# Optimization experiments

Hardware: AMD Instinct MI355X
Metric: run time of the kernel (lower is better)

Reference implementation:

```python
import jax, jax.numpy as jnp
import numpy as np
from jax import lax

PAD_IDX = 0  # padding_index from init
B, T, E, H, V = 128, 24, 512, 512, 10000


def setup_inputs() -> dict:
    key = jax.random.key(0)
    ks = jax.random.split(key, 10)
    return {
        "images": jax.random.normal(ks[0], (B, H), jnp.float32),
        "captions": jax.random.randint(ks[1], (B, T), 0, V),
        "captions_length": jax.random.randint(ks[2], (B,), 1, T + 1),
        "W_emb": jax.random.normal(ks[3], (V, E), jnp.float32) * 0.02,
        "W_ih": jax.random.normal(ks[4], (4 * H, E), jnp.float32) * 0.02,
        "W_hh": jax.random.normal(ks[5], (4 * H, H), jnp.float32) * 0.02,
        "b_ih": jax.random.normal(ks[6], (4 * H,), jnp.float32) * 0.02,
        "b_hh": jax.random.normal(ks[7], (4 * H,), jnp.float32) * 0.02,
        "W_out": jax.random.normal(ks[8], (V, H), jnp.float32) * 0.02,
        "b_out": jax.random.normal(ks[9], (V,), jnp.float32) * 0.02,
    }


def reference(images, captions, captions_length, W_emb, W_ih, W_hh, b_ih, b_hh, W_out, b_out):
    # embedding with padding_idx: padding row forced to zero
    emb_table = W_emb.at[PAD_IDX].set(0.0)
    x = emb_table[captions]  # [B, T, E]
    bdim = images.shape[0]
    hdim = W_hh.shape[1]
    vocab = W_out.shape[0]
    bias = b_ih + b_hh

    def step(carry, xt):
        h, c = carry
        # PyTorch LSTMCell gate order: i, f, g, o
        gates = xt @ W_ih.T + h @ W_hh.T + bias  # [B, 4H]
        i, f, g, o = jnp.split(gates, 4, axis=-1)
        c = jax.nn.sigmoid(f) * c + jax.nn.sigmoid(i) * jnp.tanh(g)
        h = jax.nn.sigmoid(o) * jnp.tanh(c)
        logits = h @ W_out.T + b_out  # [B, V]
        return (h, c), logits

    c0 = jnp.zeros((bdim, hdim), images.dtype)
    _, ys = lax.scan(step, (images, c0), jnp.transpose(x, (1, 0, 2)))  # ys: [T, B, V]

    # deterministic <SOS>-like start output: one-hot at index 1, prepended at t=0
    start = jnp.zeros((vocab,), images.dtype).at[1].set(1.0)
    outputs = jnp.concatenate(
        [jnp.broadcast_to(start, (bdim, 1, vocab)), jnp.transpose(ys, (1, 0, 2))], axis=1
    )  # [B, T+1, V]
    return outputs, captions_length - 1
```

## Files before the change

kernel.cpp:

```cpp
#include <hip/hip_runtime.h>

constexpr int B_  = 128;
constexpr int T_  = 24;
constexpr int E_  = 512;
constexpr int H_  = 512;
constexpr int V_  = 10000;
constexpr int G4  = 2048;
constexpr int TP1 = 25;

typedef __attribute__((ext_vector_type(8))) short bf16x8;
typedef __attribute__((ext_vector_type(4))) short short4v;
typedef __attribute__((ext_vector_type(4))) float f32x4;

#define MFMA_16x16x32_BF16(a, b, c) __builtin_amdgcn_mfma_f32_16x16x32_bf16((a), (b), (c), 0, 0, 0)

__device__ inline unsigned short f2bf(float f) {
    unsigned int u = __float_as_uint(f);
    unsigned int r = (u + 0x7FFFu + ((u >> 16) & 1u)) >> 16;
    return (unsigned short)r;
}

__device__ inline void gl16(const unsigned short* g, unsigned short* l) {
    __builtin_amdgcn_global_load_lds(
        (const __attribute__((address_space(1))) unsigned int*)g,
        (__attribute__((address_space(3))) unsigned int*)l, 16, 0, 0);
}

__device__ inline int swz16(int row, int lq) {
    return (((row << 2) | lq) ^ (row & 7)) << 3;
}

__global__ __launch_bounds__(256) void k_prep(const float* __restrict__ Wih,
                                              const float* __restrict__ Whh,
                                              const float* __restrict__ Wout,
                                              const float* __restrict__ images,
                                              const float* __restrict__ Wemb,
                                              const int* __restrict__ captions,
                                              const int* __restrict__ cap_len,
                                              unsigned short* __restrict__ dWih,
                                              unsigned short* __restrict__ dWhh,
                                              unsigned short* __restrict__ dWout,
                                              unsigned short* __restrict__ dimg,
                                              unsigned short* __restrict__ Xemb,
                                              float* __restrict__ out,
                                              unsigned* __restrict__ flg) {
    int b = blockIdx.x;
    if (b == 0) flg[threadIdx.x * 32] = 0u;
    if (b < 7112) {
        const float* src; unsigned short* dst; int i;
        if (b < 1024)      { src = Wih;    dst = dWih;  i = b * 256 + threadIdx.x; }
        else if (b < 2048) { src = Whh;    dst = dWhh;  i = (b - 1024) * 256 + threadIdx.x; }
        else if (b < 7048) { src = Wout;   dst = dWout; i = (b - 2048) * 256 + threadIdx.x; }
        else               { src = images; dst = dimg;  i = (b - 7048) * 256 + threadIdx.x; }
        float4 v = ((const float4*)src)[i];
        short4v o;
        o[0] = (short)f2bf(v.x); o[1] = (short)f2bf(v.y);
        o[2] = (short)f2bf(v.z); o[3] = (short)f2bf(v.w);
        ((short4v*)dst)[i] = o;
    } else if (b < 8648) {
        int i = (b - 7112) * 256 + threadIdx.x;
        int row = i >> 7;
        int k4  = i & 127;
        int bb = row & 127, t = row >> 7;
        int tok = captions[bb * T_ + t];
        short4v o = {0, 0, 0, 0};
        if (tok > 0 && tok < V_) {
            float4 v = ((const float4*)(Wemb + (long)tok * E_))[k4];
            o[0] = (short)f2bf(v.x); o[1] = (short)f2bf(v.y);
            o[2] = (short)f2bf(v.z); o[3] = (short)f2bf(v.w);
        }
        ((short4v*)Xemb)[(long)row * 128 + k4] = o;
    } else {
        int idx = (b - 8648) * 256 + threadIdx.x;
        constexpr int Q = V_ / 4;
        if (idx < B_ * Q) {
            int bb = idx / Q;
            int q = idx - bb * Q;
            float4 zero = {0.f, 0.f, 0.f, 0.f};
            float4 one1 = {0.f, 1.f, 0.f, 0.f};
            ((float4*)out)[(long)bb * (TP1 * Q) + q] = (q == 0) ? one1 : zero;
        }
        if (idx < B_)
            out[(size_t)B_ * TP1 * V_ + idx] = (float)(cap_len[idx] - 1);
    }
}

__global__ __launch_bounds__(256, 1) void k_lstm(const unsigned short* __restrict__ Xemb,
                                                 const unsigned short* __restrict__ h0,
                                                 unsigned* __restrict__ hx0,
                                                 unsigned* __restrict__ hx1,
                                                 unsigned short* __restrict__ Hall,
                                                 const unsigned short* __restrict__ Whh,
                                                 const unsigned short* __restrict__ Wih,
                                                 const float* __restrict__ bih,
                                                 const float* __restrict__ bhh,
                                                 unsigned* __restrict__ flg) {
    __shared__ float part[16][4][64];
    int w    = threadIdx.x >> 6;
    int lane = threadIdx.x & 63;
    int lm = lane & 15, lq = lane >> 4;
    int MI = blockIdx.x >> 5;
    int HG = blockIdx.x & 31;
    int hcol = HG * 16 + lm;
    int ks = w * 128;
    int brow = MI * 16 + lq * 4 + w;
    unsigned* myFlg = flg + (MI * 32 + HG) * 32;
    unsigned* wFlg  = flg + (MI * 32 + (w << 3)) * 32;

    bf16x8 bw[4][4];
    bf16x8 wv[4][4];
    #pragma unroll
    for (int g = 0; g < 4; g++)
        #pragma unroll
        for (int kk = 0; kk < 4; kk++) {
            size_t off = (size_t)(g * 512 + hcol) * 512 + ks + kk * 32 + lq * 8;
            bw[g][kk] = *(const bf16x8*)((const short*)Whh + off);
            wv[g][kk] = *(const bf16x8*)((const short*)Wih + off);
        }

    float bs0 = bih[0 * 512 + hcol] + bhh[0 * 512 + hcol];
    float bs1 = bih[1 * 512 + hcol] + bhh[1 * 512 + hcol];
    float bs2 = bih[2 * 512 + hcol] + bhh[2 * 512 + hcol];
    float bs3 = bih[3 * 512 + hcol] + bhh[3 * 512 + hcol];

    float cp = 0.f;

    for (int t = 0; t < T_; t++) {
        const unsigned short* X = Xemb + ((size_t)(t * 128 + MI * 16 + lm)) * 512 + ks;
        bf16x8 xa[4];
        #pragma unroll
        for (int kk = 0; kk < 4; kk++)
            xa[kk] = *(const bf16x8*)(X + kk * 32 + lq * 8);

        f32x4 acc[4] = {};
        #pragma unroll
        for (int kk = 0; kk < 4; kk++) {
            acc[0] = MFMA_16x16x32_BF16(xa[kk], wv[0][kk], acc[0]);
            acc[1] = MFMA_16x16x32_BF16(xa[kk], wv[1][kk], acc[1]);
            acc[2] = MFMA_16x16x32_BF16(xa[kk], wv[2][kk], acc[2]);
            acc[3] = MFMA_16x16x32_BF16(xa[kk], wv[3][kk], acc[3]);
        }

        bf16x8 a[4];
        if (t == 0) {
            const unsigned short* A = h0 + (size_t)(MI * 16 + lm) * 512 + ks;
            #pragma unroll
            for (int kk = 0; kk < 4; kk++)
                a[kk] = *(const bf16x8*)(A + kk * 32 + lq * 8);
        } else {
            if (lane < 8) {
                unsigned want = (unsigned)t;
                while (__hip_atomic_load(wFlg + lane * 32, __ATOMIC_RELAXED,
                                         __HIP_MEMORY_SCOPE_AGENT) < want)
                    __builtin_amdgcn_s_sleep(1);
            }
            __builtin_amdgcn_wave_barrier();
            asm volatile("" ::: "memory");
            const unsigned long long* A = (const unsigned long long*)
                (((t & 1) ? hx1 : hx0) + ((size_t)(MI * 16 + lm) * 512 + ks) / 2);
            #pragma unroll
            for (int kk = 0; kk < 4; kk++) {
                union { unsigned long long q[2]; bf16x8 v; } cv;
                cv.q[0] = __hip_atomic_load(A + kk * 8 + lq * 2,
                                            __ATOMIC_RELAXED, __HIP_MEMORY_SCOPE_AGENT);
                cv.q[1] = __hip_atomic_load(A + kk * 8 + lq * 2 + 1,
                                            __ATOMIC_RELAXED, __HIP_MEMORY_SCOPE_AGENT);
                a[kk] = cv.v;
            }
        }

        #pragma unroll
        for (int kk = 0; kk < 4; kk++) {
            acc[0] = MFMA_16x16x32_BF16(a[kk], bw[0][kk], acc[0]);
            acc[1] = MFMA_16x16x32_BF16(a[kk], bw[1][kk], acc[1]);
            acc[2] = MFMA_16x16x32_BF16(a[kk], bw[2][kk], acc[2]);
            acc[3] = MFMA_16x16x32_BF16(a[kk], bw[3][kk], acc[3]);
        }

        #pragma unroll
        for (int g = 0; g < 4; g++)
            #pragma unroll
            for (int r = 0; r < 4; r++)
                part[g * 4 + r][w][lane] = acc[g][r];
        __syncthreads();

        float gi = part[0*4+w][0][lane] + part[0*4+w][1][lane] + part[0*4+w][2][lane] + part[0*4+w][3][lane] + bs0;
        float gf = part[1*4+w][0][lane] + part[1*4+w][1][lane] + part[1*4+w][2][lane] + part[1*4+w][3][lane] + bs1;
        float gg = part[2*4+w][0][lane] + part[2*4+w][1][lane] + part[2*4+w][2][lane] + part[2*4+w][3][lane] + bs2;
        float go = part[3*4+w][0][lane] + part[3*4+w][1][lane] + part[3*4+w][2][lane] + part[3*4+w][3][lane] + bs3;
        float si = 1.f / (1.f + expf(-gi));
        float sf = 1.f / (1.f + expf(-gf));
        float so = 1.f / (1.f + expf(-go));
        float cn = sf * cp + si * tanhf(gg);
        float hn = so * tanhf(cn);
        cp = cn;
        unsigned short hb = f2bf(hn);

        if (t < T_ - 1) {
            unsigned up = ((unsigned)(unsigned short)__shfl_down((int)hb, 1) << 16) | (unsigned)hb;
            unsigned* HW = (t & 1) ? hx0 : hx1;
            if (!(lm & 1))
                __hip_atomic_store(HW + (brow * 512 + hcol) / 2, up,
                                   __ATOMIC_RELAXED, __HIP_MEMORY_SCOPE_AGENT);
            asm volatile("s_waitcnt vmcnt(0)" ::: "memory");
            __syncthreads();
            if (threadIdx.x == 0)
                __hip_atomic_store(myFlg, (unsigned)(t + 1), __ATOMIC_RELAXED,
                                   __HIP_MEMORY_SCOPE_AGENT);
        }
        Hall[(size_t)t * (B_ * H_) + brow * 512 + hcol] = hb;
    }
}

__global__ __launch_bounds__(256) void k_logits(const unsigned short* __restrict__ Hall,
                                                const unsigned short* __restrict__ Wout,
                                                const float* __restrict__ bout,
                                                float* __restrict__ out) {
    __shared__ unsigned short ldsA[2][4096];
    __shared__ unsigned short ldsB[2][4096];
    int bid = blockIdx.x;
    int xcd = bid & 7;
    int q   = bid >> 3;
    int MI  = xcd * 3 + (q % 3);
    int NI  = q / 3;
    int i    = threadIdx.x;
    int w = i >> 6, lane = i & 63;
    int lm = lane & 15, lq = lane >> 4;
    int wr = w >> 1, wc = w & 1;

    int mm0 = ((i >> 2) & 7) ^ ((i >> 4) & 1);
    int li  = i ^ mm0;
    const unsigned short* gA = Hall + (size_t)(MI * 128 + (li >> 2)) * 512 + (li & 3) * 8;
    const unsigned short* gB = Wout + (size_t)(NI * 128 + (li >> 2)) * 512 + (li & 3) * 8;
    unsigned short* lA = &ldsA[0][0] + i * 8;
    unsigned short* lB = &ldsB[0][0] + i * 8;

    auto stage = [&](int buf, int ks) {
        int go = ks * 32;
        gl16(gA + go,            lA + buf * 4096);
        gl16(gA + go + 64 * 512, lA + buf * 4096 + 2048);
        gl16(gB + go,            lB + buf * 4096);
        gl16(gB + go + 64 * 512, lB + buf * 4096 + 2048);
    };

    f32x4 acc[4][4] = {};
    stage(0, 0);
    for (int ksi = 0; ksi < 16; ksi++) {
        int cur = ksi & 1;
        if (ksi < 15) stage(cur ^ 1, ksi + 1);
        __syncthreads();
        bf16x8 af[4], bfr[4];
        #pragma unroll
        for (int mi = 0; mi < 4; mi++)
            af[mi] = *(const bf16x8*)&ldsA[cur][swz16(wr * 64 + mi * 16 + lm, lq)];
        #pragma unroll
        for (int ni = 0; ni < 4; ni++)
            bfr[ni] = *(const bf16x8*)&ldsB[cur][swz16(wc * 64 + ni * 16 + lm, lq)];
        #pragma unroll
        for (int mi = 0; mi < 4; mi++)
            #pragma unroll
            for (int ni = 0; ni < 4; ni++)
                acc[mi][ni] = MFMA_16x16x32_BF16(af[mi], bfr[ni], acc[mi][ni]);
        __syncthreads();
    }

    #pragma unroll
    for (int mi = 0; mi < 4; mi++) {
        #pragma unroll
        for (int r = 0; r < 4; r++) {
            int b = wr * 64 + mi * 16 + lq * 4 + r;
            float* orow = out + ((size_t)b * TP1 + MI + 1) * V_;
            #pragma unroll
            for (int ni = 0; ni < 4; ni++) {
                int n = NI * 128 + wc * 64 + ni * 16 + lm;
                if (n < V_) orow[n] = acc[mi][ni][r] + bout[n];
            }
        }
    }
}

extern "C" void kernel_launch(void* const* d_in, const int* in_sizes, int n_in,
                              void* d_out, int out_size, void* d_ws, size_t ws_size,
                              hipStream_t stream) {
    const float* images   = (const float*)d_in[0];
    const int*   captions = (const int*)d_in[1];
    const int*   cap_len  = (const int*)d_in[2];
    const float* Wemb     = (const float*)d_in[3];
    const float* Wih      = (const float*)d_in[4];
    const float* Whh      = (const float*)d_in[5];
    const float* bih      = (const float*)d_in[6];
    const float* bhh      = (const float*)d_in[7];
    const float* Wout     = (const float*)d_in[8];
    const float* bout     = (const float*)d_in[9];
    float* out = (float*)d_out;

    char* ws = (char*)d_ws;
    unsigned short* Wih_bf  = (unsigned short*)(ws);
    unsigned short* Whh_bf  = (unsigned short*)(ws + 2097152);
    unsigned short* Wout_bf = (unsigned short*)(ws + 4194304);
    unsigned short* Xemb    = (unsigned short*)(ws + 14434304);
    unsigned short* Hall    = (unsigned short*)(ws + 17580032);
    unsigned short* h0      = (unsigned short*)(ws + 20725760);
    unsigned*       hx0     = (unsigned*)(ws + 20856832);
    unsigned*       hx1     = (unsigned*)(ws + 20987904);
    unsigned*       flg     = (unsigned*)(ws + 21118976);

    k_prep<<<9898, 256, 0, stream>>>(Wih, Whh, Wout, images, Wemb, captions,
                                     cap_len, Wih_bf, Whh_bf, Wout_bf, h0,
                                     Xemb, out, flg);

    k_lstm<<<256, 256, 0, stream>>>(Xemb, h0, hx0, hx1, Hall, Whh_bf, Wih_bf,
                                    bih, bhh, flg);

    k_logits<<<1896, 256, 0, stream>>>(Hall, Wout_bf, bout, out);
}
```

Baseline: 319.2 us.

## Replace per-block flag barrier with step-tagged hidden-state words

```diff
diff --git a/kernel.cpp b/kernel.cpp
--- a/kernel.cpp
+++ b/kernel.cpp
@@ -43,9 +43,8 @@
                                               unsigned short* __restrict__ dimg,
                                               unsigned short* __restrict__ Xemb,
                                               float* __restrict__ out,
-                                              unsigned* __restrict__ flg) {
+                                              unsigned long long* __restrict__ hq) {
     int b = blockIdx.x;
-    if (b == 0) flg[threadIdx.x * 32] = 0u;
     if (b < 7112) {
         const float* src; unsigned short* dst; int i;
         if (b < 1024)      { src = Wih;    dst = dWih;  i = b * 256 + threadIdx.x; }
@@ -70,7 +69,7 @@
             o[2] = (short)f2bf(v.z); o[3] = (short)f2bf(v.w);
         }
         ((short4v*)Xemb)[(long)row * 128 + k4] = o;
-    } else {
+    } else if (b < 9898) {
         int idx = (b - 8648) * 256 + threadIdx.x;
         constexpr int Q = V_ / 4;
         if (idx < B_ * Q) {
@@ -82,19 +81,21 @@
         }
         if (idx < B_)
             out[(size_t)B_ * TP1 * V_ + idx] = (float)(cap_len[idx] - 1);
+    } else {
+        int idx = (b - 9898) * 256 + threadIdx.x;
+        unsigned long long* p = hq + (size_t)idx * 4;
+        p[0] = 0ull; p[1] = 0ull; p[2] = 0ull; p[3] = 0ull;
     }
 }
 
 __global__ __launch_bounds__(256, 1) void k_lstm(const unsigned short* __restrict__ Xemb,
                                                  const unsigned short* __restrict__ h0,
-                                                 unsigned* __restrict__ hx0,
-                                                 unsigned* __restrict__ hx1,
+                                                 unsigned long long* __restrict__ hq,
                                                  unsigned short* __restrict__ Hall,
                                                  const unsigned short* __restrict__ Whh,
                                                  const unsigned short* __restrict__ Wih,
                                                  const float* __restrict__ bih,
-                                                 const float* __restrict__ bhh,
-                                                 unsigned* __restrict__ flg) {
+                                                 const float* __restrict__ bhh) {
     __shared__ float part[16][4][64];
     int w    = threadIdx.x >> 6;
     int lane = threadIdx.x & 63;
@@ -104,8 +105,6 @@
     int hcol = HG * 16 + lm;
     int ks = w * 128;
     int brow = MI * 16 + lq * 4 + w;
-    unsigned* myFlg = flg + (MI * 32 + HG) * 32;
-    unsigned* wFlg  = flg + (MI * 32 + (w << 3)) * 32;
 
     bf16x8 bw[4][4];
     bf16x8 wv[4][4];
@@ -148,23 +147,30 @@
             for (int kk = 0; kk < 4; kk++)
                 a[kk] = *(const bf16x8*)(A + kk * 32 + lq * 8);
         } else {
-            if (lane < 8) {
-                unsigned want = (unsigned)t;
-                while (__hip_atomic_load(wFlg + lane * 32, __ATOMIC_RELAXED,
-                                         __HIP_MEMORY_SCOPE_AGENT) < want)
-                    __builtin_amdgcn_s_sleep(1);
-            }
-            __builtin_amdgcn_wave_barrier();
-            asm volatile("" ::: "memory");
-            const unsigned long long* A = (const unsigned long long*)
-                (((t & 1) ? hx1 : hx0) + ((size_t)(MI * 16 + lm) * 512 + ks) / 2);
+            const unsigned long long* S = hq + (size_t)(t - 1) * 32768 +
+                (size_t)(MI * 16 + lm) * 256 + (ks >> 1) + lq * 4;
+            unsigned long long q[4][4];
+            #pragma unroll
+            for (int kk = 0; kk < 4; kk++)
+                #pragma unroll
+                for (int j = 0; j < 4; j++)
+                    q[kk][j] = __hip_atomic_load(S + kk * 16 + j,
+                                 __ATOMIC_RELAXED, __HIP_MEMORY_SCOPE_AGENT);
+            unsigned want = (unsigned)t;
+            #pragma unroll
+            for (int kk = 0; kk < 4; kk++)
+                #pragma unroll
+                for (int j = 0; j < 4; j++)
+                    while ((unsigned)(q[kk][j] >> 32) != want) {
+                        __builtin_amdgcn_s_sleep(1);
+                        q[kk][j] = __hip_atomic_load(S + kk * 16 + j,
+                                     __ATOMIC_RELAXED, __HIP_MEMORY_SCOPE_AGENT);
+                    }
             #pragma unroll
             for (int kk = 0; kk < 4; kk++) {
-                union { unsigned long long q[2]; bf16x8 v; } cv;
-                cv.q[0] = __hip_atomic_load(A + kk * 8 + lq * 2,
-                                            __ATOMIC_RELAXED, __HIP_MEMORY_SCOPE_AGENT);
-                cv.q[1] = __hip_atomic_load(A + kk * 8 + lq * 2 + 1,
-                                            __ATOMIC_RELAXED, __HIP_MEMORY_SCOPE_AGENT);
+                union { unsigned u[4]; bf16x8 v; } cv;
+                #pragma unroll
+                for (int j = 0; j < 4; j++) cv.u[j] = (unsigned)q[kk][j];
                 a[kk] = cv.v;
             }
         }
@@ -197,18 +203,17 @@
         unsigned short hb = f2bf(hn);
 
         if (t < T_ - 1) {
-            unsigned up = ((unsigned)(unsigned short)__shfl_down((int)hb, 1) << 16) | (unsigned)hb;
-            unsigned* HW = (t & 1) ? hx0 : hx1;
-            if (!(lm & 1))
-                __hip_atomic_store(HW + (brow * 512 + hcol) / 2, up,
+            unsigned hb1 = (unsigned short)__shfl_down((int)hb, 1);
+            if (!(lm & 1)) {
+                unsigned long long qv = ((unsigned long long)(unsigned)(t + 1) << 32)
+                                      | ((unsigned)hb | (hb1 << 16));
+                __hip_atomic_store(hq + (size_t)t * 32768 +
+                                   ((size_t)brow * 512 + hcol) / 2, qv,
                                    __ATOMIC_RELAXED, __HIP_MEMORY_SCOPE_AGENT);
-            asm volatile("s_waitcnt vmcnt(0)" ::: "memory");
-            __syncthreads();
-            if (threadIdx.x == 0)
-                __hip_atomic_store(myFlg, (unsigned)(t + 1), __ATOMIC_RELAXED,
-                                   __HIP_MEMORY_SCOPE_AGENT);
+            }
         }
         Hall[(size_t)t * (B_ * H_) + brow * 512 + hcol] = hb;
+        __syncthreads();
     }
 }
 
@@ -295,22 +300,20 @@
     float* out = (float*)d_out;
 
     char* ws = (char*)d_ws;
-    unsigned short* Wih_bf  = (unsigned short*)(ws);
-    unsigned short* Whh_bf  = (unsigned short*)(ws + 2097152);
-    unsigned short* Wout_bf = (unsigned short*)(ws + 4194304);
-    unsigned short* Xemb    = (unsigned short*)(ws + 14434304);
-    unsigned short* Hall    = (unsigned short*)(ws + 17580032);
-    unsigned short* h0      = (unsigned short*)(ws + 20725760);
-    unsigned*       hx0     = (unsigned*)(ws + 20856832);
-    unsigned*       hx1     = (unsigned*)(ws + 20987904);
-    unsigned*       flg     = (unsigned*)(ws + 21118976);
-
-    k_prep<<<9898, 256, 0, stream>>>(Wih, Whh, Wout, images, Wemb, captions,
-                                     cap_len, Wih_bf, Whh_bf, Wout_bf, h0,
-                                     Xemb, out, flg);
-
-    k_lstm<<<256, 256, 0, stream>>>(Xemb, h0, hx0, hx1, Hall, Whh_bf, Wih_bf,
-                                    bih, bhh, flg);
+    unsigned short*     Wih_bf  = (unsigned short*)(ws);
+    unsigned short*     Whh_bf  = (unsigned short*)(ws + 2097152);
+    unsigned short*     Wout_bf = (unsigned short*)(ws + 4194304);
+    unsigned short*     Xemb    = (unsigned short*)(ws + 14434304);
+    unsigned short*     Hall    = (unsigned short*)(ws + 17580032);
+    unsigned short*     h0      = (unsigned short*)(ws + 20725760);
+    unsigned long long* hq      = (unsigned long long*)(ws + 20856832);
+
+    k_prep<<<10634, 256, 0, stream>>>(Wih, Whh, Wout, images, Wemb, captions,
+                                      cap_len, Wih_bf, Whh_bf, Wout_bf, h0,
+                                      Xemb, out, hq);
+
+    k_lstm<<<256, 256, 0, stream>>>(Xemb, h0, hq, Hall, Whh_bf, Wih_bf,
+                                    bih, bhh);
 
     k_logits<<<1896, 256, 0, stream>>>(Hall, Wout_bf, bout, out);
 }
```

Result: no change. 322.1 us (+0.9%).

## Fuse LSTM recurrence and logits GEMM into one persistent kernel with tile queue

Applied to the files above, without the earlier changes.

```diff
diff --git a/kernel.cpp b/kernel.cpp
--- a/kernel.cpp
+++ b/kernel.cpp
@@ -7,6 +7,7 @@
 constexpr int V_  = 10000;
 constexpr int G4  = 2048;
 constexpr int TP1 = 25;
+constexpr int NTILES = 1896;
 
 typedef __attribute__((ext_vector_type(8))) short bf16x8;
 typedef __attribute__((ext_vector_type(4))) short short4v;
@@ -43,9 +44,15 @@
                                               unsigned short* __restrict__ dimg,
                                               unsigned short* __restrict__ Xemb,
                                               float* __restrict__ out,
-                                              unsigned* __restrict__ flg) {
+                                              unsigned* __restrict__ flg,
+                                              unsigned* __restrict__ cnt,
+                                              int* __restrict__ queue) {
     int b = blockIdx.x;
-    if (b == 0) flg[threadIdx.x * 32] = 0u;
+    if (b == 0) {
+        flg[threadIdx.x * 32] = 0u;
+        if (threadIdx.x < 192) cnt[threadIdx.x * 32] = 0u;
+        if (threadIdx.x == 0) queue[0] = 0;
+    }
     if (b < 7112) {
         const float* src; unsigned short* dst; int i;
         if (b < 1024)      { src = Wih;    dst = dWih;  i = b * 256 + threadIdx.x; }
@@ -85,7 +92,7 @@
     }
 }
 
-__global__ __launch_bounds__(256, 1) void k_lstm(const unsigned short* __restrict__ Xemb,
+__global__ __launch_bounds__(256, 3) void k_main(const unsigned short* __restrict__ Xemb,
                                                  const unsigned short* __restrict__ h0,
                                                  unsigned* __restrict__ hx0,
                                                  unsigned* __restrict__ hx1,
@@ -94,186 +101,214 @@
                                                  const unsigned short* __restrict__ Wih,
                                                  const float* __restrict__ bih,
                                                  const float* __restrict__ bhh,
-                                                 unsigned* __restrict__ flg) {
-    __shared__ float part[16][4][64];
-    int w    = threadIdx.x >> 6;
-    int lane = threadIdx.x & 63;
-    int lm = lane & 15, lq = lane >> 4;
-    int MI = blockIdx.x >> 5;
-    int HG = blockIdx.x & 31;
-    int hcol = HG * 16 + lm;
-    int ks = w * 128;
-    int brow = MI * 16 + lq * 4 + w;
-    unsigned* myFlg = flg + (MI * 32 + HG) * 32;
-    unsigned* wFlg  = flg + (MI * 32 + (w << 3)) * 32;
-
-    bf16x8 bw[4][4];
-    bf16x8 wv[4][4];
-    #pragma unroll
-    for (int g = 0; g < 4; g++)
-        #pragma unroll
-        for (int kk = 0; kk < 4; kk++) {
-            size_t off = (size_t)(g * 512 + hcol) * 512 + ks + kk * 32 + lq * 8;
-            bw[g][kk] = *(const bf16x8*)((const short*)Whh + off);
-            wv[g][kk] = *(const bf16x8*)((const short*)Wih + off);
-        }
-
-    float bs0 = bih[0 * 512 + hcol] + bhh[0 * 512 + hcol];
-    float bs1 = bih[1 * 512 + hcol] + bhh[1 * 512 + hcol];
-    float bs2 = bih[2 * 512 + hcol] + bhh[2 * 512 + hcol];
-    float bs3 = bih[3 * 512 + hcol] + bhh[3 * 512 + hcol];
-
-    float cp = 0.f;
-
-    for (int t = 0; t < T_; t++) {
-        const unsigned short* X = Xemb + ((size_t)(t * 128 + MI * 16 + lm)) * 512 + ks;
-        bf16x8 xa[4];
-        #pragma unroll
-        for (int kk = 0; kk < 4; kk++)
-            xa[kk] = *(const bf16x8*)(X + kk * 32 + lq * 8);
-
-        f32x4 acc[4] = {};
-        #pragma unroll
-        for (int kk = 0; kk < 4; kk++) {
-            acc[0] = MFMA_16x16x32_BF16(xa[kk], wv[0][kk], acc[0]);
-            acc[1] = MFMA_16x16x32_BF16(xa[kk], wv[1][kk], acc[1]);
-            acc[2] = MFMA_16x16x32_BF16(xa[kk], wv[2][kk], acc[2]);
-            acc[3] = MFMA_16x16x32_BF16(xa[kk], wv[3][kk], acc[3]);
-        }
-
-        bf16x8 a[4];
-        if (t == 0) {
-            const unsigned short* A = h0 + (size_t)(MI * 16 + lm) * 512 + ks;
-            #pragma unroll
-            for (int kk = 0; kk < 4; kk++)
-                a[kk] = *(const bf16x8*)(A + kk * 32 + lq * 8);
-        } else {
-            if (lane < 8) {
-                unsigned want = (unsigned)t;
-                while (__hip_atomic_load(wFlg + lane * 32, __ATOMIC_RELAXED,
-                                         __HIP_MEMORY_SCOPE_AGENT) < want)
-                    __builtin_amdgcn_s_sleep(1);
-            }
-            __builtin_amdgcn_wave_barrier();
-            asm volatile("" ::: "memory");
-            const unsigned long long* A = (const unsigned long long*)
-                (((t & 1) ? hx1 : hx0) + ((size_t)(MI * 16 + lm) * 512 + ks) / 2);
-            #pragma unroll
-            for (int kk = 0; kk < 4; kk++) {
-                union { unsigned long long q[2]; bf16x8 v; } cv;
-                cv.q[0] = __hip_atomic_load(A + kk * 8 + lq * 2,
-                                            __ATOMIC_RELAXED, __HIP_MEMORY_SCOPE_AGENT);
-                cv.q[1] = __hip_atomic_load(A + kk * 8 + lq * 2 + 1,
-                                            __ATOMIC_RELAXED, __HIP_MEMORY_SCOPE_AGENT);
-                a[kk] = cv.v;
-            }
-        }
-
-        #pragma unroll
-        for (int kk = 0; kk < 4; kk++) {
-            acc[0] = MFMA_16x16x32_BF16(a[kk], bw[0][kk], acc[0]);
-            acc[1] = MFMA_16x16x32_BF16(a[kk], bw[1][kk], acc[1]);
-            acc[2] = MFMA_16x16x32_BF16(a[kk], bw[2][kk], acc[2]);
-            acc[3] = MFMA_16x16x32_BF16(a[kk], bw[3][kk], acc[3]);
-        }
-
+                                                 unsigned* __restrict__ flg,
+                                                 unsigned* __restrict__ cnt,
+                                                 int* __restrict__ queue,
+                                                 const unsigned short* __restrict__ Wout,
+                                                 const float* __restrict__ bout,
+                                                 float* __restrict__ out) {
+    __shared__ char smem[32768];
+    __shared__ int qs;
+    unsigned* HallU = (unsigned*)Hall;
+
+    if (blockIdx.x < 256) {
+        float (*part)[4][64] = (float(*)[4][64])smem;
+        int w    = threadIdx.x >> 6;
+        int lane = threadIdx.x & 63;
+        int lm = lane & 15, lq = lane >> 4;
+        int MI = blockIdx.x >> 5;
+        int HG = blockIdx.x & 31;
+        int hcol = HG * 16 + lm;
+        int ks = w * 128;
+        int brow = MI * 16 + lq * 4 + w;
+        unsigned* myFlg = flg + (MI * 32 + HG) * 32;
+        unsigned* wFlg  = flg + (MI * 32 + (w << 3)) * 32;
+
+        bf16x8 bw[4][4], wv[4][4];
         #pragma unroll
         for (int g = 0; g < 4; g++)
             #pragma unroll
-            for (int r = 0; r < 4; r++)
-                part[g * 4 + r][w][lane] = acc[g][r];
-        __syncthreads();
-
-        float gi = part[0*4+w][0][lane] + part[0*4+w][1][lane] + part[0*4+w][2][lane] + part[0*4+w][3][lane] + bs0;
-        float gf = part[1*4+w][0][lane] + part[1*4+w][1][lane] + part[1*4+w][2][lane] + part[1*4+w][3][lane] + bs1;
-        float gg = part[2*4+w][0][lane] + part[2*4+w][1][lane] + part[2*4+w][2][lane] + part[2*4+w][3][lane] + bs2;
-        float go = part[3*4+w][0][lane] + part[3*4+w][1][lane] + part[3*4+w][2][lane] + part[3*4+w][3][lane] + bs3;
-        float si = 1.f / (1.f + expf(-gi));
-        float sf = 1.f / (1.f + expf(-gf));
-        float so = 1.f / (1.f + expf(-go));
-        float cn = sf * cp + si * tanhf(gg);
-        float hn = so * tanhf(cn);
-        cp = cn;
-        unsigned short hb = f2bf(hn);
-
-        if (t < T_ - 1) {
-            unsigned up = ((unsigned)(unsigned short)__shfl_down((int)hb, 1) << 16) | (unsigned)hb;
-            unsigned* HW = (t & 1) ? hx0 : hx1;
-            if (!(lm & 1))
-                __hip_atomic_store(HW + (brow * 512 + hcol) / 2, up,
-                                   __ATOMIC_RELAXED, __HIP_MEMORY_SCOPE_AGENT);
+            for (int kk = 0; kk < 4; kk++) {
+                size_t off = (size_t)(g * 512 + hcol) * 512 + ks + kk * 32 + lq * 8;
+                bw[g][kk] = *(const bf16x8*)((const short*)Whh + off);
+                wv[g][kk] = *(const bf16x8*)((const short*)Wih + off);
+            }
+        float bs0 = bih[0 * 512 + hcol] + bhh[0 * 512 + hcol];
+        float bs1 = bih[1 * 512 + hcol] + bhh[1 * 512 + hcol];
+        float bs2 = bih[2 * 512 + hcol] + bhh[2 * 512 + hcol];
+        float bs3 = bih[3 * 512 + hcol] + bhh[3 * 512 + hcol];
+        float cp = 0.f;
+
+        for (int t = 0; t < T_; t++) {
+            const unsigned short* X = Xemb + ((size_t)(t * 128 + MI * 16 + lm)) * 512 + ks;
+            bf16x8 xa[4];
+            #pragma unroll
+            for (int kk = 0; kk < 4; kk++)
+                xa[kk] = *(const bf16x8*)(X + kk * 32 + lq * 8);
+
+            f32x4 acc[4] = {};
+            #pragma unroll
+            for (int kk = 0; kk < 4; kk++) {
+                acc[0] = MFMA_16x16x32_BF16(xa[kk], wv[0][kk], acc[0]);
+                acc[1] = MFMA_16x16x32_BF16(xa[kk], wv[1][kk], acc[1]);
+                acc[2] = MFMA_16x16x32_BF16(xa[kk], wv[2][kk], acc[2]);
+                acc[3] = MFMA_16x16x32_BF16(xa[kk], wv[3][kk], acc[3]);
+            }
+
+            bf16x8 a[4];
+            if (t == 0) {
+                const unsigned short* A = h0 + (size_t)(MI * 16 + lm) * 512 + ks;
+                #pragma unroll
+                for (int kk = 0; kk < 4; kk++)
+                    a[kk] = *(const bf16x8*)(A + kk * 32 + lq * 8);
+            } else {
+                if (lane < 8) {
+                    unsigned want = (unsigned)t;
+                    while (__hip_atomic_load(wFlg + lane * 32, __ATOMIC_RELAXED,
+                                             __HIP_MEMORY_SCOPE_AGENT) < want)
+                        __builtin_amdgcn_s_sleep(1);
+                }
+                __builtin_amdgcn_wave_barrier();
+                asm volatile("" ::: "memory");
+                const unsigned long long* A = (const unsigned long long*)
+                    (((t & 1) ? hx1 : hx0) + ((size_t)(MI * 16 + lm) * 512 + ks) / 2);
+                #pragma unroll
+                for (int kk = 0; kk < 4; kk++) {
+                    union { unsigned long long q[2]; bf16x8 v; } cv;
+                    cv.q[0] = __hip_atomic_load(A + kk * 8 + lq * 2,
+                                                __ATOMIC_RELAXED, __HIP_MEMORY_SCOPE_AGENT);
+                    cv.q[1] = __hip_atomic_load(A + kk * 8 + lq * 2 + 1,
+                                                __ATOMIC_RELAXED, __HIP_MEMORY_SCOPE_AGENT);
+                    a[kk] = cv.v;
+                }
+            }
+
+            #pragma unroll
+            for (int kk = 0; kk < 4; kk++) {
+                acc[0] = MFMA_16x16x32_BF16(a[kk], bw[0][kk], acc[0]);
+                acc[1] = MFMA_16x16x32_BF16(a[kk], bw[1][kk], acc[1]);
+                acc[2] = MFMA_16x16x32_BF16(a[kk], bw[2][kk], acc[2]);
+                acc[3] = MFMA_16x16x32_BF16(a[kk], bw[3][kk], acc[3]);
+            }
+
+            #pragma unroll
+            for (int g = 0; g < 4; g++)
+                #pragma unroll
+                for (int r = 0; r < 4; r++)
+                    part[g * 4 + r][w][lane] = acc[g][r];
+            __syncthreads();
+
+            float gi = part[0*4+w][0][lane] + part[0*4+w][1][lane] + part[0*4+w][2][lane] + part[0*4+w][3][lane] + bs0;
+            float gf = part[1*4+w][0][lane] + part[1*4+w][1][lane] + part[1*4+w][2][lane] + part[1*4+w][3][lane] + bs1;
+            float gg = part[2*4+w][0][lane] + part[2*4+w][1][lane] + part[2*4+w][2][lane] + part[2*4+w][3][lane] + bs2;
+            float go = part[3*4+w][0][lane] + part[3*4+w][1][lane] + part[3*4+w][2][lane] + part[3*4+w][3][lane] + bs3;
+            float si = 1.f / (1.f + expf(-gi));
+            float sf = 1.f / (1.f + expf(-gf));
+            float so = 1.f / (1.f + expf(-go));
+            float cn = sf * cp + si * tanhf(gg);
+            float hn = so * tanhf(cn);
+            cp = cn;
+            unsigned short hb = f2bf(hn);
+
+            unsigned hb1 = (unsigned short)__shfl_down((int)hb, 1);
+            unsigned pv = (unsigned)hb | (hb1 << 16);
+            if (!(lm & 1)) {
+                if (t < T_ - 1) {
+                    unsigned* HW = (t & 1) ? hx0 : hx1;
+                    __hip_atomic_store(HW + (brow * 512 + hcol) / 2, pv,
+                                       __ATOMIC_RELAXED, __HIP_MEMORY_SCOPE_AGENT);
+                }
+                __hip_atomic_store(HallU + ((size_t)t * 65536 + (size_t)brow * 512 + hcol) / 2,
+                                   pv, __ATOMIC_RELAXED, __HIP_MEMORY_SCOPE_AGENT);
+            }
             asm volatile("s_waitcnt vmcnt(0)" ::: "memory");
             __syncthreads();
-            if (threadIdx.x == 0)
-                __hip_atomic_store(myFlg, (unsigned)(t + 1), __ATOMIC_RELAXED,
-                                   __HIP_MEMORY_SCOPE_AGENT);
+            if (threadIdx.x == 0) {
+                if (t < T_ - 1)
+                    __hip_atomic_store(myFlg, (unsigned)(t + 1), __ATOMIC_RELAXED,
+                                       __HIP_MEMORY_SCOPE_AGENT);
+                __hip_atomic_fetch_add(cnt + ((t << 3) + MI) * 32, 1u,
+                                       __ATOMIC_RELAXED, __HIP_MEMORY_SCOPE_AGENT);
+            }
         }
-        Hall[(size_t)t * (B_ * H_) + brow * 512 + hcol] = hb;
-    }
-}
-
-__global__ __launch_bounds__(256) void k_logits(const unsigned short* __restrict__ Hall,
-                                                const unsigned short* __restrict__ Wout,
-                                                const float* __restrict__ bout,
-                                                float* __restrict__ out) {
-    __shared__ unsigned short ldsA[2][4096];
-    __shared__ unsigned short ldsB[2][4096];
-    int bid = blockIdx.x;
-    int xcd = bid & 7;
-    int q   = bid >> 3;
-    int MI  = xcd * 3 + (q % 3);
-    int NI  = q / 3;
-    int i    = threadIdx.x;
-    int w = i >> 6, lane = i & 63;
-    int lm = lane & 15, lq = lane >> 4;
-    int wr = w >> 1, wc = w & 1;
-
-    int mm0 = ((i >> 2) & 7) ^ ((i >> 4) & 1);
-    int li  = i ^ mm0;
-    const unsigned short* gA = Hall + (size_t)(MI * 128 + (li >> 2)) * 512 + (li & 3) * 8;
-    const unsigned short* gB = Wout + (size_t)(NI * 128 + (li >> 2)) * 512 + (li & 3) * 8;
-    unsigned short* lA = &ldsA[0][0] + i * 8;
-    unsigned short* lB = &ldsB[0][0] + i * 8;
-
-    auto stage = [&](int buf, int ks) {
-        int go = ks * 32;
-        gl16(gA + go,            lA + buf * 4096);
-        gl16(gA + go + 64 * 512, lA + buf * 4096 + 2048);
-        gl16(gB + go,            lB + buf * 4096);
-        gl16(gB + go + 64 * 512, lB + buf * 4096 + 2048);
-    };
-
-    f32x4 acc[4][4] = {};
-    stage(0, 0);
-    for (int ksi = 0; ksi < 16; ksi++) {
-        int cur = ksi & 1;
-        if (ksi < 15) stage(cur ^ 1, ksi + 1);
-        __syncthreads();
-        bf16x8 af[4], bfr[4];
-        #pragma unroll
-        for (int mi = 0; mi < 4; mi++)
-            af[mi] = *(const bf16x8*)&ldsA[cur][swz16(wr * 64 + mi * 16 + lm, lq)];
-        #pragma unroll
-        for (int ni = 0; ni < 4; ni++)
-            bfr[ni] = *(const bf16x8*)&ldsB[cur][swz16(wc * 64 + ni * 16 + lm, lq)];
-        #pragma unroll
-        for (int mi = 0; mi < 4; mi++)
-            #pragma unroll
-            for (int ni = 0; ni < 4; ni++)
-                acc[mi][ni] = MFMA_16x16x32_BF16(af[mi], bfr[ni], acc[mi][ni]);
         __syncthreads();
     }
 
-    #pragma unroll
-    for (int mi = 0; mi < 4; mi++) {
-        #pragma unroll
-        for (int r = 0; r < 4; r++) {
-            int b = wr * 64 + mi * 16 + lq * 4 + r;
-            float* orow = out + ((size_t)b * TP1 + MI + 1) * V_;
-            #pragma unroll
-            for (int ni = 0; ni < 4; ni++) {
-                int n = NI * 128 + wc * 64 + ni * 16 + lm;
-                if (n < V_) orow[n] = acc[mi][ni][r] + bout[n];
+    {
+        unsigned short* ldsA0 = (unsigned short*)smem;
+        unsigned short* ldsB0 = (unsigned short*)(smem + 16384);
+        int i = threadIdx.x;
+        int w = i >> 6, lane = i & 63;
+        int lm = lane & 15, lq = lane >> 4;
+        int wr = w >> 1, wc = w & 1;
+        int mm0 = ((i >> 2) & 7) ^ ((i >> 4) & 1);
+        int li  = i ^ mm0;
+        unsigned short* lA = ldsA0 + i * 8;
+        unsigned short* lB = ldsB0 + i * 8;
+
+        for (;;) {
+            if (threadIdx.x == 0) qs = atomicAdd(queue, 1);
+            __syncthreads();
+            int q = qs;
+            if (q >= NTILES) break;
+            int MI = q / 79;
+            int NI = q - MI * 79;
+
+            if (threadIdx.x < 8) {
+                while (__hip_atomic_load(cnt + ((MI << 3) + threadIdx.x) * 32,
+                                         __ATOMIC_RELAXED, __HIP_MEMORY_SCOPE_AGENT) < 32u)
+                    __builtin_amdgcn_s_sleep(16);
+            }
+            __syncthreads();
+
+            const unsigned short* gA = Hall + (size_t)(MI * 128 + (li >> 2)) * 512 + (li & 3) * 8;
+            const unsigned short* gB = Wout + (size_t)(NI * 128 + (li >> 2)) * 512 + (li & 3) * 8;
+
+            f32x4 acc[4][4] = {};
+            {
+                gl16(gA,            lA);
+                gl16(gA + 64 * 512, lA + 2048);
+                gl16(gB,            lB);
+                gl16(gB + 64 * 512, lB + 2048);
+            }
+            for (int ksi = 0; ksi < 16; ksi++) {
+                int cur = ksi & 1;
+                if (ksi < 15) {
+                    int go = (ksi + 1) * 32;
+                    int bo = (cur ^ 1) * 4096;
+                    gl16(gA + go,            lA + bo);
+                    gl16(gA + go + 64 * 512, lA + bo + 2048);
+                    gl16(gB + go,            lB + bo);
+                    gl16(gB + go + 64 * 512, lB + bo + 2048);
+                }
+                __syncthreads();
+                bf16x8 af[4], bfr[4];
+                #pragma unroll
+                for (int mi = 0; mi < 4; mi++)
+                    af[mi] = *(const bf16x8*)&ldsA0[cur * 4096 + swz16(wr * 64 + mi * 16 + lm, lq)];
+                #pragma unroll
+                for (int ni = 0; ni < 4; ni++)
+                    bfr[ni] = *(const bf16x8*)&ldsB0[cur * 4096 + swz16(wc * 64 + ni * 16 + lm, lq)];
+                #pragma unroll
+                for (int mi = 0; mi < 4; mi++)
+                    #pragma unroll
+                    for (int ni = 0; ni < 4; ni++)
+                        acc[mi][ni] = MFMA_16x16x32_BF16(af[mi], bfr[ni], acc[mi][ni]);
+                __syncthreads();
+            }
+
+            #pragma unroll
+            for (int mi = 0; mi < 4; mi++) {
+                #pragma unroll
+                for (int r = 0; r < 4; r++) {
+                    int b = wr * 64 + mi * 16 + lq * 4 + r;
+                    float* orow = out + ((size_t)b * TP1 + MI + 1) * V_;
+                    #pragma unroll
+                    for (int ni = 0; ni < 4; ni++) {
+                        int n = NI * 128 + wc * 64 + ni * 16 + lm;
+                        if (n < V_) orow[n] = acc[mi][ni][r] + bout[n];
+                    }
+                }
             }
         }
     }
@@ -304,13 +339,14 @@
     unsigned*       hx0     = (unsigned*)(ws + 20856832);
     unsigned*       hx1     = (unsigned*)(ws + 20987904);
     unsigned*       flg     = (unsigned*)(ws + 21118976);
+    unsigned*       cnt     = (unsigned*)(ws + 21151744);
+    int*            queue   = (int*)(ws + 21176320);
 
     k_prep<<<9898, 256, 0, stream>>>(Wih, Whh, Wout, images, Wemb, captions,
                                      cap_len, Wih_bf, Whh_bf, Wout_bf, h0,
-                                     Xemb, out, flg);
-
-    k_lstm<<<256, 256, 0, stream>>>(Xemb, h0, hx0, hx1, Hall, Whh_bf, Wih_bf,
-                                    bih, bhh, flg);
-
-    k_logits<<<1896, 256, 0, stream>>>(Hall, Wout_bf, bout, out);
-}
+                                     Xemb, out, flg, cnt, queue);
+
+    k_main<<<768, 256, 0, stream>>>(Xemb, h0, hx0, hx1, Hall, Whh_bf, Wih_bf,
+                                    bih, bhh, flg, cnt, queue,
+                                    Wout_bf, bout, out);
+}
```

Result: slower. 404.6 us (+26.8%).
